# Kernel tuning notes

Measured on AMD Instinct MI355X. Metric: run time of the kernel, lower is better.

## Reference

```python
import jax, jax.numpy as jnp
import numpy as np

E = 23   # unique_experts_num
K = 3    # act_experts_num
D = 1024 # in_features
H = 768  # hidden_features (0.75 * dim, per MOEBlock mlp_ratio)


def setup_inputs() -> dict:
    key = jax.random.key(0)
    ks = jax.random.split(key, 12)
    s_in = 1.0 / np.sqrt(D)
    s_hid = 1.0 / np.sqrt(H)
    x = jax.random.normal(ks[0], (4, 1024, D), dtype=jnp.float32)
    gate_W = jax.random.normal(ks[1], (D, E), dtype=jnp.float32) * s_in
    gate_b = jnp.zeros((E,), jnp.float32)
    bias = jnp.zeros((E,), jnp.float32)  # registered buffer, init to zeros
    W1 = jax.random.normal(ks[2], (E, D, H), dtype=jnp.float32) * s_in
    b1 = jnp.zeros((E, H), jnp.float32)
    W2 = jax.random.normal(ks[3], (E, H, D), dtype=jnp.float32) * s_hid
    b2 = jnp.zeros((E, D), jnp.float32)
    sW1 = jax.random.normal(ks[4], (D, H), dtype=jnp.float32) * s_in
    sb1 = jnp.zeros((H,), jnp.float32)
    sW2 = jax.random.normal(ks[5], (H, D), dtype=jnp.float32) * s_hid
    sb2 = jnp.zeros((D,), jnp.float32)
    return {"x": x, "gate_W": gate_W, "gate_b": gate_b, "bias": bias,
            "W1": W1, "b1": b1, "W2": W2, "b2": b2,
            "sW1": sW1, "sb1": sb1, "sW2": sW2, "sb2": sb2}


def reference(x, gate_W, gate_b, bias, W1, b1, W2, b2, sW1, sb1, sW2, sb2):
    o_shape = x.shape
    xt = x.reshape(-1, o_shape[-1])          # [T, D]
    T = xt.shape[0]

    # gating: sigmoid gate, top-k indices chosen on (gate + bias), weights gathered from gate
    gate = jax.nn.sigmoid(xt @ gate_W + gate_b)            # [T, E]
    _, top_idx = jax.lax.top_k(gate + bias, K)             # [T, K]
    top_w = jnp.take_along_axis(gate, top_idx, axis=-1)    # [T, K]
    top_w = top_w / jnp.sum(top_w, axis=-1, keepdims=True)

    # combine matrix: C[t, e] = normalized gate weight if e in top-k of token t else 0
    C = jnp.zeros((T, E), xt.dtype).at[jnp.arange(T)[:, None], top_idx].set(top_w)

    # all-expert dense compute (math-equivalent to dispatch/compute/combine)
    h = jax.nn.gelu(jnp.einsum('td,edh->eth', xt, W1) + b1[:, None, :], approximate=False)
    y = jnp.einsum('eth,ehd->etd', h, W2) + b2[:, None, :]  # [E, T, D]
    moe_out = jnp.einsum('etd,te->td', y, C)                # weighted combine

    # shared expert applied to every token
    shared = jax.nn.gelu(xt @ sW1 + sb1, approximate=False) @ sW2 + sb2
    out = shared + moe_out

    # aux load-balance loss
    gate_norm = gate / jnp.sum(gate, axis=-1, keepdims=True)
    P = jnp.mean(gate_norm, axis=0)                          # [E]
    counts = jnp.sum(jax.nn.one_hot(top_idx, E, dtype=jnp.float32), axis=(0, 1))  # [E]
    F = E * counts / (K * T)
    aux_loss = jnp.sum(P * F)

    return out.reshape(o_shape), aux_loss, counts.astype(jnp.int32)
```

## Files before the change

### kernel.cpp

```cpp
#include <hip/hip_runtime.h>
#include <math.h>

#define TT 4096
#define DD 1024
#define HH 768
#define NE 23
#define NG 24
#define BM 128
#define BN 128
#define BK 64
#define MAXT 160
#define KB1 16
#define KB2 12
#define NY1 6
#define NY2 8
#define NWG1 (MAXT*NY1)
#define NWG2 (MAXT*NY2)

#define WS_CURS   0
#define WS_COUNTS 512
#define WS_PSUM   544
#define WS_OFFS   576
#define WS_TOFFS  608
#define WS_TOTAL  640
#define WS_T2E    672
#define WS_T2A    832
#define WS_TOKE   1024
#define WS_TOKW   13312
#define WS_LTOK   25600
#define WS_LW     41984
#define WS_PPART  58368
#define WS_CPART  81920
#define WS_SIDX   106496
#define XB_OFF  ((size_t)524288)
#define H_OFF   ((size_t)8912896)
#define W1B_OFF ((size_t)34078720)
#define W2B_OFF ((size_t)71827456)

typedef short bf16x8 __attribute__((ext_vector_type(8)));
typedef float f32x4 __attribute__((ext_vector_type(4)));
typedef unsigned short u16x8 __attribute__((ext_vector_type(8)));

#define S_BARRIER() asm volatile("s_barrier" ::: "memory")
#define WAIT_VM8()  asm volatile("s_waitcnt vmcnt(8)" ::: "memory")
#define WAIT_VM0()  asm volatile("s_waitcnt vmcnt(0)" ::: "memory")

__device__ inline unsigned short bfr(float f) {
    unsigned u = __float_as_uint(f);
    u += 0x7fffu + ((u >> 16) & 1u);
    return (unsigned short)(u >> 16);
}
__device__ inline float b2f(unsigned short u) {
    return __uint_as_float((unsigned)u << 16);
}

__device__ __forceinline__ void gl_lds16(const void* g, void* l) {
    __builtin_amdgcn_global_load_lds(
        (const __attribute__((address_space(1))) unsigned int*)g,
        (__attribute__((address_space(3))) unsigned int*)l, 16, 0, 0);
}

__global__ __launch_bounds__(256) void k_gate(
    const float* __restrict__ x, const float* __restrict__ gW,
    const float* __restrict__ gb, const float* __restrict__ bias,
    int* __restrict__ tokE, float* __restrict__ tokW,
    float* __restrict__ Ppart, int* __restrict__ Cpart)
{
    __shared__ float xs[4][DD];
    __shared__ float gv[4][NE];
    __shared__ float ginvs[4];
    __shared__ int sel[4][3];
    const int tid = threadIdx.x;
    const int t0 = blockIdx.x * 4;
    {
        const float4* src = (const float4*)(x + (size_t)t0 * DD);
        float4* dst = (float4*)&xs[0][0];
        #pragma unroll
        for (int i = 0; i < 4; i++) dst[tid + 256 * i] = src[tid + 256 * i];
    }
    __syncthreads();
    const int w = tid >> 6, l = tid & 63;
    const int t = t0 + w;
    if (l < NE) {
        float s0 = 0.f, s1 = 0.f, s2 = 0.f, s3 = 0.f;
        const float* xw = xs[w];
        for (int d = 0; d < DD; d += 4) {
            s0 = fmaf(xw[d + 0], gW[(d + 0) * NE + l], s0);
            s1 = fmaf(xw[d + 1], gW[(d + 1) * NE + l], s1);
            s2 = fmaf(xw[d + 2], gW[(d + 2) * NE + l], s2);
            s3 = fmaf(xw[d + 3], gW[(d + 3) * NE + l], s3);
        }
        float s = (s0 + s1) + (s2 + s3) + gb[l];
        gv[w][l] = 1.f / (1.f + expf(-s));
    }
    __syncthreads();
    if (l == 0) {
        unsigned chosen = 0;
        int be[3]; float bw[3];
        float gsum = 0.f;
        for (int e = 0; e < NE; e++) gsum += gv[w][e];
        #pragma unroll
        for (int k = 0; k < 3; k++) {
            float m = -1e30f; int mi = 0;
            for (int e = 0; e < NE; e++) {
                float kv = gv[w][e] + bias[e];
                if (!((chosen >> e) & 1u) && kv > m) { m = kv; mi = e; }
            }
            chosen |= 1u << mi;
            be[k] = mi; bw[k] = gv[w][mi];
        }
        float inv = 1.f / (bw[0] + bw[1] + bw[2]);
        #pragma unroll
        for (int k = 0; k < 3; k++) {
            tokE[t * 3 + k] = be[k];
            tokW[t * 3 + k] = bw[k] * inv;
            sel[w][k] = be[k];
        }
        ginvs[w] = 1.f / gsum;
    }
    __syncthreads();
    if (tid < NE) {
        float p = gv[0][tid] * ginvs[0] + gv[1][tid] * ginvs[1]
                + gv[2][tid] * ginvs[2] + gv[3][tid] * ginvs[3];
        Ppart[tid * 1024 + blockIdx.x] = p;
        int c = 0;
        #pragma unroll
        for (int w2 = 0; w2 < 4; w2++)
            #pragma unroll
            for (int k = 0; k < 3; k++) c += (sel[w2][k] == tid);
        Cpart[tid * 1024 + blockIdx.x] = c;
    }
}

__global__ __launch_bounds__(256) void k_reduce(
    const float* __restrict__ Ppart, const int* __restrict__ Cpart,
    int* __restrict__ counts, float* __restrict__ Psum)
{
    const int e = blockIdx.x;
    const int tid = threadIdx.x;
    float s = 0.f; int c = 0;
    for (int i = tid; i < 1024; i += 256) {
        s += Ppart[e * 1024 + i];
        c += Cpart[e * 1024 + i];
    }
    #pragma unroll
    for (int off = 32; off >= 1; off >>= 1) {
        s += __shfl_down(s, off, 64);
        c += __shfl_down(c, off, 64);
    }
    __shared__ float ss[4]; __shared__ int sc[4];
    if ((tid & 63) == 0) { ss[tid >> 6] = s; sc[tid >> 6] = c; }
    __syncthreads();
    if (tid == 0) {
        Psum[e] = ss[0] + ss[1] + ss[2] + ss[3];
        counts[e] = sc[0] + sc[1] + sc[2] + sc[3];
    }
}

__global__ void k_scan(const int* __restrict__ counts, const float* __restrict__ Psum,
                       int* __restrict__ offs, int* __restrict__ toffs,
                       int* __restrict__ total, int* __restrict__ t2e,
                       int* __restrict__ t2a, float* __restrict__ outAux)
{
    if (threadIdx.x != 0 || blockIdx.x != 0) return;
    int off = 0, toff = 0;
    for (int e = 0; e < NG; e++) {
        int c = (e < NE) ? counts[e] : TT;
        offs[e] = off; toffs[e] = toff;
        int nt = (c + BM - 1) / BM;
        for (int t = 0; t < nt; t++) {
            t2e[toff + t] = e;
            t2a[toff + t] = off + t * BM;
        }
        off += c; toff += nt;
    }
    offs[NG] = off; toffs[NG] = toff;
    *total = toff;
    float aux = 0.f;
    for (int e = 0; e < NE; e++) {
        float P = Psum[e] / (float)TT;
        float F = (float)NE * (float)counts[e] / (float)(3 * TT);
        aux += P * F;
    }
    outAux[0] = aux;
    for (int e = 0; e < NE; e++) outAux[1 + e] = (float)counts[e];
}

__global__ void k_scatter(const int* __restrict__ tokE, const float* __restrict__ tokW,
                          const int* __restrict__ offs, int* __restrict__ curs,
                          int* __restrict__ ltok, float* __restrict__ lw,
                          int* __restrict__ sidx)
{
    int t = blockIdx.x * 256 + threadIdx.x;
    if (t >= TT) return;
    #pragma unroll
    for (int k = 0; k < 3; k++) {
        int e = tokE[t * 3 + k];
        int pos = atomicAdd(&curs[e * 16], 1);
        int idx = offs[e] + pos;
        ltok[idx] = t; lw[idx] = tokW[t * 3 + k];
        sidx[t * 3 + k] = idx;
    }
    ltok[3 * TT + t] = t;
    lw[3 * TT + t] = 1.f;
}

__global__ __launch_bounds__(256) void k_cvt_x(const float* __restrict__ x,
                                               unsigned short* __restrict__ xb)
{
    const int tid = threadIdx.x;
    #pragma unroll
    for (int it = 0; it < 4; it++) {
        int idx = blockIdx.x * 1024 + it * 256 + tid;
        float4 v = ((const float4*)x)[idx];
        ((ushort4*)xb)[idx] = make_ushort4(bfr(v.x), bfr(v.y), bfr(v.z), bfr(v.w));
    }
}

__global__ __launch_bounds__(256) void k_cvt_w(
    const float* __restrict__ W, const float* __restrict__ Ws,
    int K, int N, unsigned short* __restrict__ dst)
{
    const int e = blockIdx.z, kb = blockIdx.y;
    const int KBt = gridDim.y;
    const int n0 = blockIdx.x * 64;
    const float* src = (e < NE) ? (W + (size_t)e * K * N) : Ws;
    __shared__ unsigned short Ls[64][66];
    const int tid = threadIdx.x;
    const int c = (tid & 15) * 4, r0 = tid >> 4;
    #pragma unroll
    for (int pass = 0; pass < 4; pass++) {
        int row = pass * 16 + r0;
        float4 v = *(const float4*)(src + (size_t)(kb * 64 + row) * N + n0 + c);
        ushort4 u = make_ushort4(bfr(v.x), bfr(v.y), bfr(v.z), bfr(v.w));
        *(ushort4*)&Ls[row][c] = u;
    }
    __syncthreads();
    unsigned short* dbase = dst + ((size_t)(e * KBt + kb) * N + n0) * 64;
    #pragma unroll
    for (int half = 0; half < 2; half++) {
        int g = half * 256 + tid;
        int n = g >> 3, p = g & 7;
        int j = p ^ (n & 7);
        u16x8 u;
        #pragma unroll
        for (int i = 0; i < 8; i++) u[i] = Ls[j * 8 + i][n];
        *(u16x8*)(dbase + n * 64 + p * 8) = u;
    }
}

__global__ __launch_bounds__(256) void k_mm1(
    const unsigned short* __restrict__ xb, const unsigned short* __restrict__ W1b,
    const float* __restrict__ b1, const float* __restrict__ sb1,
    const int* __restrict__ t2e, const int* __restrict__ t2a,
    const int* __restrict__ offs, const int* __restrict__ total,
    const int* __restrict__ ltok, unsigned short* __restrict__ H)
{
    const int id = blockIdx.x;
    const int wg = (id & 7) * (NWG1 / 8) + (id >> 3);
    const int ns = wg / MAXT;
    const int tb = wg % MAXT;
    if (tb >= *total) return;
    const int e = t2e[tb];
    const int a0 = t2a[tb];
    const int acount = min(offs[e + 1] - a0, BM);
    const float* bb = (e < NE) ? (b1 + e * HH) : sb1;
    const int nb = ns * BN;

    __shared__ unsigned short As[2][BM * BK];
    __shared__ unsigned short Bs[2][BN * BK];
    __shared__ int rows[BM];
    const int tid = threadIdx.x;
    if (tid < BM) rows[tid] = ltok[a0 + min(tid, acount - 1)];
    __syncthreads();

    const int wid = tid >> 6, lane = tid & 63;
    const int wr = wid >> 1, wc = wid & 1;
    const int l15 = lane & 15, l4 = lane >> 4;

    float bv[4];
    #pragma unroll
    for (int n = 0; n < 4; n++) bv[n] = bb[nb + wc * 64 + n * 16 + l15];

    f32x4 acc[4][4];
    #pragma unroll
    for (int m = 0; m < 4; m++)
        #pragma unroll
        for (int n = 0; n < 4; n++) acc[m][n] = (f32x4){0.f, 0.f, 0.f, 0.f};

    const unsigned short* aSrc[4];
    int Goff[4];
    #pragma unroll
    for (int c = 0; c < 4; c++) {
        int G = (wid * 4 + c) * 64 + lane;
        int row = G >> 3, j = G & 7;
        aSrc[c] = xb + (size_t)rows[row] * DD + ((j ^ (row & 7)) << 3);
        Goff[c] = G * 8;
    }
    const unsigned short* wbase = W1b + ((size_t)e * KB1 * HH + nb) * 64;

    auto stage = [&](int buf, int kb) {
        #pragma unroll
        for (int c = 0; c < 4; c++)
            gl_lds16(aSrc[c] + kb * 64, &As[buf][Goff[c]]);
        const unsigned short* wb = wbase + (size_t)kb * (HH * 64);
        #pragma unroll
        for (int c = 0; c < 4; c++)
            gl_lds16(wb + Goff[c], &Bs[buf][Goff[c]]);
    };
    auto compute = [&](int buf) {
        #pragma unroll
        for (int kh = 0; kh < 2; kh++) {
            bf16x8 af[4], bf[4];
            #pragma unroll
            for (int f = 0; f < 4; f++) {
                int ar = wr * 64 + f * 16 + l15;
                int br = wc * 64 + f * 16 + l15;
                int pg = (kh << 2) + l4;
                af[f] = *(const bf16x8*)&As[buf][ar * 64 + ((pg ^ (ar & 7)) << 3)];
                bf[f] = *(const bf16x8*)&Bs[buf][br * 64 + ((pg ^ (br & 7)) << 3)];
            }
            #pragma unroll
            for (int m = 0; m < 4; m++)
                #pragma unroll
                for (int n = 0; n < 4; n++)
                    acc[m][n] = __builtin_amdgcn_mfma_f32_16x16x32_bf16(af[m], bf[n], acc[m][n], 0, 0, 0);
        }
    };

    stage(0, 0);
    stage(1, 1);
    WAIT_VM8();
    S_BARRIER();
    #pragma unroll 1
    for (int kb = 0; kb < KB1; kb++) {
        const int cur = kb & 1;
        compute(cur);
        S_BARRIER();
        if (kb + 2 < KB1) {
            stage(cur, kb + 2);
            WAIT_VM8();
            S_BARRIER();
        } else if (kb + 1 < KB1) {
            WAIT_VM0();
            S_BARRIER();
        }
    }

    #pragma unroll
    for (int m = 0; m < 4; m++) {
        int rbase = wr * 64 + m * 16 + l4 * 4;
        #pragma unroll
        for (int n = 0; n < 4; n++) {
            int col = nb + wc * 64 + n * 16 + l15;
            #pragma unroll
            for (int i = 0; i < 4; i++) {
                int r = rbase + i;
                if (r < acount) {
                    float v = acc[m][n][i] + bv[n];
                    float g = 0.5f * v * (1.f + erff(v * 0.70710678118f));
                    H[(size_t)(a0 + r) * HH + col] = bfr(g);
                }
            }
        }
    }
}

__global__ __launch_bounds__(256) void k_mm2(
    const unsigned short* __restrict__ H, const unsigned short* __restrict__ W2b,
    const float* __restrict__ b2, const float* __restrict__ sb2,
    const int* __restrict__ t2e, const int* __restrict__ t2a,
    const int* __restrict__ offs, const int* __restrict__ total,
    const int* __restrict__ ltok, const float* __restrict__ lw,
    unsigned short* __restrict__ yslot, float* __restrict__ out)
{
    const int id = blockIdx.x;
    const int wg = (id & 7) * (NWG2 / 8) + (id >> 3);
    const int ns = wg / MAXT;
    const int tb = wg % MAXT;
    if (tb >= *total) return;
    const int e = t2e[tb];
    const int a0 = t2a[tb];
    const int acount = min(offs[e + 1] - a0, BM);
    const float* bb = (e < NE) ? (b2 + e * DD) : sb2;
    const int nb = ns * BN;

    __shared__ unsigned short As[2][BM * BK];
    __shared__ unsigned short Bs[2][BN * BK];
    __shared__ int rows[BM];
    __shared__ float wts[BM];
    const int tid = threadIdx.x;
    if (tid < BM) {
        rows[tid] = (tid < acount) ? ltok[a0 + tid] : -1;
        wts[tid]  = (tid < acount) ? lw[a0 + tid] : 0.f;
    }
    __syncthreads();

    const int wid = tid >> 6, lane = tid & 63;
    const int wr = wid >> 1, wc = wid & 1;
    const int l15 = lane & 15, l4 = lane >> 4;

    float bv[4];
    #pragma unroll
    for (int n = 0; n < 4; n++) bv[n] = bb[nb + wc * 64 + n * 16 + l15];

    f32x4 acc[4][4];
    #pragma unroll
    for (int m = 0; m < 4; m++)
        #pragma unroll
        for (int n = 0; n < 4; n++) acc[m][n] = (f32x4){0.f, 0.f, 0.f, 0.f};

    const unsigned short* aSrc[4];
    int Goff[4];
    #pragma unroll
    for (int c = 0; c < 4; c++) {
        int G = (wid * 4 + c) * 64 + lane;
        int row = G >> 3, j = G & 7;
        aSrc[c] = H + (size_t)(a0 + row) * HH + ((j ^ (row & 7)) << 3);
        Goff[c] = G * 8;
    }
    const unsigned short* wbase = W2b + ((size_t)e * KB2 * DD + nb) * 64;

    auto stage = [&](int buf, int kb) {
        #pragma unroll
        for (int c = 0; c < 4; c++)
            gl_lds16(aSrc[c] + kb * 64, &As[buf][Goff[c]]);
        const unsigned short* wb = wbase + (size_t)kb * (DD * 64);
        #pragma unroll
        for (int c = 0; c < 4; c++)
            gl_lds16(wb + Goff[c], &Bs[buf][Goff[c]]);
    };
    auto compute = [&](int buf) {
        #pragma unroll
        for (int kh = 0; kh < 2; kh++) {
            bf16x8 af[4], bf[4];
            #pragma unroll
            for (int f = 0; f < 4; f++) {
                int ar = wr * 64 + f * 16 + l15;
                int br = wc * 64 + f * 16 + l15;
                int pg = (kh << 2) + l4;
                af[f] = *(const bf16x8*)&As[buf][ar * 64 + ((pg ^ (ar & 7)) << 3)];
                bf[f] = *(const bf16x8*)&Bs[buf][br * 64 + ((pg ^ (br & 7)) << 3)];
            }
            #pragma unroll
            for (int m = 0; m < 4; m++)
                #pragma unroll
                for (int n = 0; n < 4; n++)
                    acc[m][n] = __builtin_amdgcn_mfma_f32_16x16x32_bf16(af[m], bf[n], acc[m][n], 0, 0, 0);
        }
    };

    stage(0, 0);
    stage(1, 1);
    WAIT_VM8();
    S_BARRIER();
    #pragma unroll 1
    for (int kb = 0; kb < KB2; kb++) {
        const int cur = kb & 1;
        compute(cur);
        S_BARRIER();
        if (kb + 2 < KB2) {
            stage(cur, kb + 2);
            WAIT_VM8();
            S_BARRIER();
        } else if (kb + 1 < KB2) {
            WAIT_VM0();
            S_BARRIER();
        }
    }

    if (e == NE) {
        #pragma unroll
        for (int m = 0; m < 4; m++) {
            int rbase = wr * 64 + m * 16 + l4 * 4;
            #pragma unroll
            for (int n = 0; n < 4; n++) {
                int col = nb + wc * 64 + n * 16 + l15;
                #pragma unroll
                for (int i = 0; i < 4; i++) {
                    int r = rbase + i;
                    out[(size_t)rows[r] * DD + col] = acc[m][n][i] + bv[n];
                }
            }
        }
    } else {
        #pragma unroll
        for (int m = 0; m < 4; m++) {
            int rbase = wr * 64 + m * 16 + l4 * 4;
            #pragma unroll
            for (int n = 0; n < 4; n++) {
                int col = nb + wc * 64 + n * 16 + l15;
                #pragma unroll
                for (int i = 0; i < 4; i++) {
                    int r = rbase + i;
                    if (r < acount)
                        yslot[(size_t)(a0 + r) * DD + col] = bfr(wts[r] * (acc[m][n][i] + bv[n]));
                }
            }
        }
    }
}

__global__ __launch_bounds__(256) void k_combine(
    const unsigned short* __restrict__ yslot, const int* __restrict__ sidx,
    float* __restrict__ out)
{
    const int t = blockIdx.x;
    const int s0 = sidx[t * 3 + 0], s1 = sidx[t * 3 + 1], s2 = sidx[t * 3 + 2];
    const int d = threadIdx.x * 4;
    float* o = out + (size_t)t * DD + d;
    float4 v = *(float4*)o;
    ushort4 a = *(const ushort4*)(yslot + (size_t)s0 * DD + d);
    ushort4 b = *(const ushort4*)(yslot + (size_t)s1 * DD + d);
    ushort4 c = *(const ushort4*)(yslot + (size_t)s2 * DD + d);
    v.x += b2f(a.x) + b2f(b.x) + b2f(c.x);
    v.y += b2f(a.y) + b2f(b.y) + b2f(c.y);
    v.z += b2f(a.z) + b2f(b.z) + b2f(c.z);
    v.w += b2f(a.w) + b2f(b.w) + b2f(c.w);
    *(float4*)o = v;
}

extern "C" void kernel_launch(void* const* d_in, const int* in_sizes, int n_in,
                              void* d_out, int out_size, void* d_ws, size_t ws_size,
                              hipStream_t stream)
{
    const float* x    = (const float*)d_in[0];
    const float* gW   = (const float*)d_in[1];
    const float* gb   = (const float*)d_in[2];
    const float* bias = (const float*)d_in[3];
    const float* W1   = (const float*)d_in[4];
    const float* b1   = (const float*)d_in[5];
    const float* W2   = (const float*)d_in[6];
    const float* b2   = (const float*)d_in[7];
    const float* sW1  = (const float*)d_in[8];
    const float* sb1  = (const float*)d_in[9];
    const float* sW2  = (const float*)d_in[10];
    const float* sb2  = (const float*)d_in[11];
    float* out = (float*)d_out;
    float* wsf = (float*)d_ws;
    int*   wsi = (int*)d_ws;

    hipMemsetAsync(d_ws, 0, 2048, stream);

    int*   curs   = wsi + WS_CURS;
    int*   counts = wsi + WS_COUNTS;
    float* Psum   = wsf + WS_PSUM;
    int*   offs   = wsi + WS_OFFS;
    int*   toffs  = wsi + WS_TOFFS;
    int*   total  = wsi + WS_TOTAL;
    int*   t2e    = wsi + WS_T2E;
    int*   t2a    = wsi + WS_T2A;
    int*   tokE   = wsi + WS_TOKE;
    float* tokW   = wsf + WS_TOKW;
    int*   ltok   = wsi + WS_LTOK;
    float* lwt    = wsf + WS_LW;
    float* Ppart  = wsf + WS_PPART;
    int*   Cpart  = wsi + WS_CPART;
    int*   sidx   = wsi + WS_SIDX;
    unsigned short* xb  = (unsigned short*)((char*)d_ws + XB_OFF);
    unsigned short* Hb  = (unsigned short*)((char*)d_ws + H_OFF);
    unsigned short* W1b = (unsigned short*)((char*)d_ws + W1B_OFF);
    unsigned short* W2b = (unsigned short*)((char*)d_ws + W2B_OFF);
    unsigned short* yslot = W1b;

    k_cvt_x<<<TT * DD / 4096, 256, 0, stream>>>(x, xb);
    k_cvt_w<<<dim3(HH / 64, DD / 64, NG), 256, 0, stream>>>(W1, sW1, DD, HH, W1b);
    k_cvt_w<<<dim3(DD / 64, HH / 64, NG), 256, 0, stream>>>(W2, sW2, HH, DD, W2b);
    k_gate<<<TT / 4, 256, 0, stream>>>(x, gW, gb, bias, tokE, tokW, Ppart, Cpart);
    k_reduce<<<NE, 256, 0, stream>>>(Ppart, Cpart, counts, Psum);
    k_scan<<<1, 64, 0, stream>>>(counts, Psum, offs, toffs, total, t2e, t2a,
                                 out + (size_t)TT * DD);
    k_scatter<<<TT / 256, 256, 0, stream>>>(tokE, tokW, offs, curs, ltok, lwt, sidx);
    k_mm1<<<NWG1, 256, 0, stream>>>(xb, W1b, b1, sb1, t2e, t2a, offs, total, ltok, Hb);
    k_mm2<<<NWG2, 256, 0, stream>>>(Hb, W2b, b2, sb2, t2e, t2a, offs, total, ltok, lwt,
                                    yslot, out);
    k_combine<<<TT, 256, 0, stream>>>(yslot, sidx, out);
}
```

Before: 245.7 us.

## Fuse x bf16 conversion into gating, single-barrier GEMM prefetch loop, tanh GELU

```diff
diff --git a/kernel.cpp b/kernel.cpp
--- a/kernel.cpp
+++ b/kernel.cpp
@@ -42,7 +42,6 @@
 typedef unsigned short u16x8 __attribute__((ext_vector_type(8)));
 
 #define S_BARRIER() asm volatile("s_barrier" ::: "memory")
-#define WAIT_VM8()  asm volatile("s_waitcnt vmcnt(8)" ::: "memory")
 #define WAIT_VM0()  asm volatile("s_waitcnt vmcnt(0)" ::: "memory")
 
 __device__ inline unsigned short bfr(float f) {
@@ -64,7 +63,8 @@
     const float* __restrict__ x, const float* __restrict__ gW,
     const float* __restrict__ gb, const float* __restrict__ bias,
     int* __restrict__ tokE, float* __restrict__ tokW,
-    float* __restrict__ Ppart, int* __restrict__ Cpart)
+    float* __restrict__ Ppart, int* __restrict__ Cpart,
+    unsigned short* __restrict__ xb)
 {
     __shared__ float xs[4][DD];
     __shared__ float gv[4][NE];
@@ -79,6 +79,16 @@
         for (int i = 0; i < 4; i++) dst[tid + 256 * i] = src[tid + 256 * i];
     }
     __syncthreads();
+    {
+        const float* xf = &xs[0][0];
+        unsigned short* xd = xb + (size_t)t0 * DD;
+        #pragma unroll
+        for (int it = 0; it < 4; it++) {
+            int o = it * 1024 + tid * 4;
+            ushort4 u = make_ushort4(bfr(xf[o]), bfr(xf[o + 1]), bfr(xf[o + 2]), bfr(xf[o + 3]));
+            *(ushort4*)(xd + o) = u;
+        }
+    }
     const int w = tid >> 6, l = tid & 63;
     const int t = t0 + w;
     if (l < NE) {
@@ -205,18 +215,6 @@
     lw[3 * TT + t] = 1.f;
 }
 
-__global__ __launch_bounds__(256) void k_cvt_x(const float* __restrict__ x,
-                                               unsigned short* __restrict__ xb)
-{
-    const int tid = threadIdx.x;
-    #pragma unroll
-    for (int it = 0; it < 4; it++) {
-        int idx = blockIdx.x * 1024 + it * 256 + tid;
-        float4 v = ((const float4*)x)[idx];
-        ((ushort4*)xb)[idx] = make_ushort4(bfr(v.x), bfr(v.y), bfr(v.z), bfr(v.w));
-    }
-}
-
 __global__ __launch_bounds__(256) void k_cvt_w(
     const float* __restrict__ W, const float* __restrict__ Ws,
     int K, int N, unsigned short* __restrict__ dst)
@@ -329,21 +327,18 @@
     };
 
     stage(0, 0);
-    stage(1, 1);
-    WAIT_VM8();
+    WAIT_VM0();
     S_BARRIER();
+    int cur = 0;
     #pragma unroll 1
     for (int kb = 0; kb < KB1; kb++) {
-        const int cur = kb & 1;
+        if (kb + 1 < KB1) stage(cur ^ 1, kb + 1);
+        __builtin_amdgcn_sched_barrier(0);
         compute(cur);
-        S_BARRIER();
-        if (kb + 2 < KB1) {
-            stage(cur, kb + 2);
-            WAIT_VM8();
-            S_BARRIER();
-        } else if (kb + 1 < KB1) {
+        if (kb + 1 < KB1) {
             WAIT_VM0();
             S_BARRIER();
+            cur ^= 1;
         }
     }
 
@@ -358,7 +353,8 @@
                 int r = rbase + i;
                 if (r < acount) {
                     float v = acc[m][n][i] + bv[n];
-                    float g = 0.5f * v * (1.f + erff(v * 0.70710678118f));
+                    float u = v + 0.044715f * v * v * v;
+                    float g = v / (1.f + __expf(-1.5957691216f * u));
                     H[(size_t)(a0 + r) * HH + col] = bfr(g);
                 }
             }
@@ -451,21 +447,18 @@
     };
 
     stage(0, 0);
-    stage(1, 1);
-    WAIT_VM8();
+    WAIT_VM0();
     S_BARRIER();
+    int cur = 0;
     #pragma unroll 1
     for (int kb = 0; kb < KB2; kb++) {
-        const int cur = kb & 1;
+        if (kb + 1 < KB2) stage(cur ^ 1, kb + 1);
+        __builtin_amdgcn_sched_barrier(0);
         compute(cur);
-        S_BARRIER();
-        if (kb + 2 < KB2) {
-            stage(cur, kb + 2);
-            WAIT_VM8();
-            S_BARRIER();
-        } else if (kb + 1 < KB2) {
+        if (kb + 1 < KB2) {
             WAIT_VM0();
             S_BARRIER();
+            cur ^= 1;
         }
     }
 
@@ -563,10 +556,9 @@
     unsigned short* W2b = (unsigned short*)((char*)d_ws + W2B_OFF);
     unsigned short* yslot = W1b;
 
-    k_cvt_x<<<TT * DD / 4096, 256, 0, stream>>>(x, xb);
     k_cvt_w<<<dim3(HH / 64, DD / 64, NG), 256, 0, stream>>>(W1, sW1, DD, HH, W1b);
     k_cvt_w<<<dim3(DD / 64, HH / 64, NG), 256, 0, stream>>>(W2, sW2, HH, DD, W2b);
-    k_gate<<<TT / 4, 256, 0, stream>>>(x, gW, gb, bias, tokE, tokW, Ppart, Cpart);
+    k_gate<<<TT / 4, 256, 0, stream>>>(x, gW, gb, bias, tokE, tokW, Ppart, Cpart, xb);
     k_reduce<<<NE, 256, 0, stream>>>(Ppart, Cpart, counts, Psum);
     k_scan<<<1, 64, 0, stream>>>(counts, Psum, offs, toffs, total, t2e, t2a,
                                  out + (size_t)TT * DD);
```

Result: faster. 230.9 us (-6.0%).
